# Kernel tuning notes

Hardware: AMD Instinct MI355X
Metric: run time of the kernel (lower is better)

The kernel has to match this reference:

```python
import jax, jax.numpy as jnp
import numpy as np

NUM_NODES = 50000
NUM_RELATIONS = 16
HIDDEN_DIM = 256
NUM_EDGES = 800000


def setup_inputs() -> dict:
    key = jax.random.key(0)
    k_x, k_ei, k_et, k_wr, k_ws, k_b = jax.random.split(key, 6)
    x = jax.random.normal(k_x, (NUM_NODES, HIDDEN_DIM), dtype=jnp.float32)
    edge_index = jax.random.randint(k_ei, (2, NUM_EDGES), 0, NUM_NODES, dtype=jnp.int64)
    edge_type = jax.random.randint(k_et, (NUM_EDGES,), 0, NUM_RELATIONS, dtype=jnp.int64)
    # Xavier-uniform-like scale for relation weights (fan_in=fan_out=d)
    lim = float(np.sqrt(6.0 / (HIDDEN_DIM + HIDDEN_DIM)))
    W_rel = jax.random.uniform(k_wr, (NUM_RELATIONS, HIDDEN_DIM, HIDDEN_DIM), minval=-lim, maxval=lim, dtype=jnp.float32)
    W_self = jax.random.uniform(k_ws, (HIDDEN_DIM, HIDDEN_DIM), minval=-lim, maxval=lim, dtype=jnp.float32)
    bias = jnp.zeros((HIDDEN_DIM,), dtype=jnp.float32)
    return {"x": x, "edge_index": edge_index, "edge_type": edge_type,
            "W_rel": W_rel, "W_self": W_self, "bias": bias}


def reference(x, edge_index, edge_type, W_rel, W_self, bias):
    # Transform every node under every relation: (N, R, d)
    xw = jnp.einsum('nd,rdh->nrh', x, W_rel)
    src = edge_index[0]
    dst = edge_index[1]
    # Per-edge messages: gather the (src, relation)-specific transform. (E, d)
    messages = xw[src, edge_type]
    # Scatter-add into destination nodes (sum over relations is implicit since
    # each edge carries exactly one relation and sums commute).
    agg = jax.ops.segment_sum(messages, dst, num_segments=NUM_NODES)
    out = agg + x @ W_self + bias
    return jax.nn.relu(out)
```

## Files before the change

kernel.cpp:

```cpp
#include <hip/hip_runtime.h>
#include <hip/hip_bf16.h>
#include <stdint.h>

#define D 256

typedef __attribute__((ext_vector_type(8))) short bf16x8;
typedef __attribute__((ext_vector_type(4))) float f32x4;
typedef __attribute__((ext_vector_type(4))) unsigned int u32x4;

#define GLOBAL_AS __attribute__((address_space(1)))
#define LDS_AS __attribute__((address_space(3)))

__device__ __forceinline__ unsigned short f2bf(float f) {
  union { float f; unsigned int u; } c; c.f = f;
  unsigned int r = (c.u + 0x7fffu + ((c.u >> 16) & 1u)) >> 16;
  return (unsigned short)r;
}
__device__ __forceinline__ float bf2f(unsigned short h) {
  union { unsigned int u; float f; } c; c.u = ((unsigned int)h) << 16;
  return c.f;
}

__global__ void convert_x_kernel(const float* __restrict__ x,
                                 unsigned short* __restrict__ xb, int n4) {
  int i = blockIdx.x * blockDim.x + threadIdx.x;
  if (i >= n4) return;
  float4 v = reinterpret_cast<const float4*>(x)[i];
  ushort4 o;
  o.x = f2bf(v.x); o.y = f2bf(v.y); o.z = f2bf(v.z); o.w = f2bf(v.w);
  reinterpret_cast<ushort4*>(xb)[i] = o;
}

__global__ void transpose_w_kernel(const float* __restrict__ Wrel,
                                   const float* __restrict__ Wself,
                                   unsigned short* __restrict__ Wt, int R) {
  __shared__ unsigned short tile[64][65];
  int r = blockIdx.z;
  const float* src = (r == R) ? Wself : (Wrel + (size_t)r * D * D);
  int d0 = blockIdx.x * 64, h0 = blockIdx.y * 64;
  for (int i = threadIdx.x; i < 64 * 64; i += blockDim.x) {
    int row = i >> 6, col = i & 63;
    tile[row][col] = f2bf(src[(size_t)(d0 + row) * D + h0 + col]);
  }
  __syncthreads();
  for (int i = threadIdx.x; i < 64 * 64; i += blockDim.x) {
    int row = i >> 6, col = i & 63;
    Wt[(size_t)r * D * D + (size_t)(h0 + row) * D + d0 + col] = tile[col][row];
  }
}

template <int MODE, int XB>
__global__ __launch_bounds__(256) void gemm_kernel(
    const unsigned short* __restrict__ Abf,
    const float* __restrict__ Af,
    const unsigned short* __restrict__ Bt,
    unsigned short* __restrict__ Cbf,
    float* __restrict__ Cf,
    const float* __restrict__ bias, int M, int ldc, int ntiles) {
  __shared__ unsigned short smem[128 * 128];
  unsigned short* As = smem;
  unsigned short* Bs = smem + 8192;

  const int tid = threadIdx.x;
  const int lane = tid & 63;
  const int wid = tid >> 6;
  const int wm = wid >> 1, wn = wid & 1;

  const int MBt = (M + 127) >> 7;
  const int PANEL = 8;
  const int per_panel = PANEL * ntiles;
  const int panel = blockIdx.x / per_panel;
  const int rem = blockIdx.x - panel * per_panel;
  const int pm0 = panel * PANEL;
  const int ph = min(PANEL, MBt - pm0);
  const int mi = pm0 + rem % ph;
  const int ni = rem / ph;
  const int m0 = mi * 128;
  const int n0 = ni * 128;

  f32x4 acc[4][4] = {};

  for (int k0 = 0; k0 < 256; k0 += 64) {
    __syncthreads();
    for (int i = 0; i < 4; ++i) {
      int chunk = i * 4 + wid;
      int row = chunk * 8 + (lane >> 3);
      int col = (lane & 7) * 8;
      const unsigned short* gb = Bt + (size_t)(n0 + row) * 256 + k0 + col;
      __builtin_amdgcn_global_load_lds((GLOBAL_AS void*)(void*)gb,
                                       (LDS_AS void*)(Bs + chunk * 512), 16, 0, 0);
    }
    if (XB) {
      for (int i = 0; i < 4; ++i) {
        int chunk = i * 4 + wid;
        int row = chunk * 8 + (lane >> 3);
        int col = (lane & 7) * 8;
        int ar = m0 + row; if (ar > M - 1) ar = M - 1;
        const unsigned short* ga = Abf + (size_t)ar * 256 + k0 + col;
        __builtin_amdgcn_global_load_lds((GLOBAL_AS void*)(void*)ga,
                                         (LDS_AS void*)(As + chunk * 512), 16, 0, 0);
      }
    } else {
      for (int i = 0; i < 8; ++i) {
        int idx = i * 256 + tid;
        int row = idx >> 4;
        int c4 = idx & 15;
        int ar = m0 + row; if (ar > M - 1) ar = M - 1;
        float4 v = *reinterpret_cast<const float4*>(Af + (size_t)ar * 256 + k0 + c4 * 4);
        ushort4 o;
        o.x = f2bf(v.x); o.y = f2bf(v.y); o.z = f2bf(v.z); o.w = f2bf(v.w);
        *reinterpret_cast<ushort4*>(&As[row * 64 + c4 * 4]) = o;
      }
    }
    __syncthreads();
    for (int kk = 0; kk < 2; ++kk) {
      bf16x8 af[4], bfr[4];
      int kof = kk * 32 + (lane >> 4) * 8;
      for (int mi2 = 0; mi2 < 4; ++mi2)
        af[mi2] = *(const bf16x8*)&As[(wm * 64 + mi2 * 16 + (lane & 15)) * 64 + kof];
      for (int ni2 = 0; ni2 < 4; ++ni2)
        bfr[ni2] = *(const bf16x8*)&Bs[(wn * 64 + ni2 * 16 + (lane & 15)) * 64 + kof];
      for (int mi2 = 0; mi2 < 4; ++mi2)
        for (int ni2 = 0; ni2 < 4; ++ni2)
          acc[mi2][ni2] = __builtin_amdgcn_mfma_f32_16x16x32_bf16(
              af[mi2], bfr[ni2], acc[mi2][ni2], 0, 0, 0);
    }
  }

  if (MODE == 1) {
    for (int mi2 = 0; mi2 < 4; ++mi2)
      for (int ni2 = 0; ni2 < 4; ++ni2) {
        int col = n0 + wn * 64 + ni2 * 16 + (lane & 15);
        int rbase = m0 + wm * 64 + mi2 * 16 + (lane >> 4) * 4;
        float b = bias[col];
        for (int j = 0; j < 4; ++j) {
          int row = rbase + j;
          if (row < M) Cf[(size_t)row * 256 + col] = acc[mi2][ni2][j] + b;
        }
      }
  } else {
    __syncthreads();
    for (int mi2 = 0; mi2 < 4; ++mi2)
      for (int ni2 = 0; ni2 < 4; ++ni2) {
        int colt = wn * 64 + ni2 * 16 + (lane & 15);
        int rbt = wm * 64 + mi2 * 16 + (lane >> 4) * 4;
        for (int j = 0; j < 4; ++j)
          smem[(rbt + j) * 128 + colt] = f2bf(acc[mi2][ni2][j]);
      }
    __syncthreads();
    for (int i = 0; i < 8; ++i) {
      int c = i * 256 + tid;
      int row = c >> 4;
      int cole = (c & 15) * 8;
      int grow = m0 + row;
      if (grow < M)
        *(u32x4*)&Cbf[(size_t)grow * ldc + n0 + cole] =
            *(const u32x4*)&smem[row * 128 + cole];
    }
  }
}

__global__ void hist_kernel(const int* __restrict__ ei, const int* __restrict__ et,
                            int* __restrict__ counts, int E, int M, int R, int RB) {
  for (int i = blockIdx.x * blockDim.x + threadIdx.x; i < E;
       i += gridDim.x * blockDim.x) {
    int dst = min(max(ei[E + i], 0), M - 1);
    int rel = min(max(et[i], 0), R - 1);
    int b = rel / RB;
    atomicAdd(&counts[b * M + dst], 1);
  }
}

__global__ void scan1_kernel(const int* __restrict__ counts, int* __restrict__ bsum,
                             int NBINS) {
  __shared__ int red[256];
  int i = blockIdx.x * 256 + threadIdx.x;
  red[threadIdx.x] = (i < NBINS) ? counts[i] : 0;
  __syncthreads();
  for (int s = 128; s > 0; s >>= 1) {
    if (threadIdx.x < s) red[threadIdx.x] += red[threadIdx.x + s];
    __syncthreads();
  }
  if (threadIdx.x == 0) bsum[blockIdx.x] = red[0];
}

__global__ void scan2_kernel(int* __restrict__ bsum, int NB) {
  __shared__ int sh[1024];
  int t = threadIdx.x;
  int v = (t < NB) ? bsum[t] : 0;
  sh[t] = v;
  __syncthreads();
  for (int off = 1; off < 1024; off <<= 1) {
    int u = (t >= off) ? sh[t - off] : 0;
    __syncthreads();
    sh[t] += u;
    __syncthreads();
  }
  if (t < NB) bsum[t] = sh[t] - v;
}

__global__ void scan3_kernel(const int* __restrict__ counts, const int* __restrict__ bsum,
                             int* __restrict__ offs, int NBINS) {
  __shared__ int sh[256];
  int b = blockIdx.x, t = threadIdx.x;
  int i = b * 256 + t;
  int v = (i < NBINS) ? counts[i] : 0;
  sh[t] = v;
  __syncthreads();
  for (int off = 1; off < 256; off <<= 1) {
    int u = (t >= off) ? sh[t - off] : 0;
    __syncthreads();
    sh[t] += u;
    __syncthreads();
  }
  int excl = sh[t] - v + bsum[b];
  if (i < NBINS) offs[i] = excl;
  if (i == NBINS - 1) offs[NBINS] = excl + v;
}

__global__ void fill_kernel(const int* __restrict__ ei, const int* __restrict__ et,
                            const int* __restrict__ offs, int* __restrict__ cursor,
                            int* __restrict__ ev, int E, int M, int R, int RB) {
  for (int i = blockIdx.x * blockDim.x + threadIdx.x; i < E;
       i += gridDim.x * blockDim.x) {
    int dst = min(max(ei[E + i], 0), M - 1);
    int src = min(max(ei[i], 0), M - 1);
    int rel = min(max(et[i], 0), R - 1);
    int b = rel / RB;
    int bin = b * M + dst;
    int p = atomicAdd(&cursor[bin], 1);
    ev[offs[bin] + p] = src * RB + (rel - b * RB);
  }
}

template <int RELU>
__global__ void gather_kernel(const int* __restrict__ offs, const int* __restrict__ ev,
                              const unsigned short* __restrict__ xw,
                              float* __restrict__ out, int M, int base) {
  int w = blockIdx.x * (blockDim.x >> 6) + (threadIdx.x >> 6);
  int lane = threadIdx.x & 63;
  if (w >= M) return;
  int beg = offs[base + w], end = offs[base + w + 1];
  float a0 = 0, a1 = 0, a2 = 0, a3 = 0;
  int s = beg;
  for (; s + 3 < end; s += 4) {
    int v0 = ev[s], v1 = ev[s + 1], v2 = ev[s + 2], v3 = ev[s + 3];
    ushort4 t0 = *((const ushort4*)(xw + ((size_t)v0 << 8)) + lane);
    ushort4 t1 = *((const ushort4*)(xw + ((size_t)v1 << 8)) + lane);
    ushort4 t2 = *((const ushort4*)(xw + ((size_t)v2 << 8)) + lane);
    ushort4 t3 = *((const ushort4*)(xw + ((size_t)v3 << 8)) + lane);
    a0 += bf2f(t0.x) + bf2f(t1.x) + bf2f(t2.x) + bf2f(t3.x);
    a1 += bf2f(t0.y) + bf2f(t1.y) + bf2f(t2.y) + bf2f(t3.y);
    a2 += bf2f(t0.z) + bf2f(t1.z) + bf2f(t2.z) + bf2f(t3.z);
    a3 += bf2f(t0.w) + bf2f(t1.w) + bf2f(t2.w) + bf2f(t3.w);
  }
  for (; s < end; ++s) {
    int v = ev[s];
    ushort4 t = *((const ushort4*)(xw + ((size_t)v << 8)) + lane);
    a0 += bf2f(t.x); a1 += bf2f(t.y); a2 += bf2f(t.z); a3 += bf2f(t.w);
  }
  if (RELU || end > beg) {
    float4* o = (float4*)(out + (size_t)w * 256) + lane;
    float4 cur = *o;
    cur.x += a0; cur.y += a1; cur.z += a2; cur.w += a3;
    if (RELU) {
      cur.x = fmaxf(cur.x, 0.f); cur.y = fmaxf(cur.y, 0.f);
      cur.z = fmaxf(cur.z, 0.f); cur.w = fmaxf(cur.w, 0.f);
    }
    *o = cur;
  }
}

__global__ void relu_kernel(float* __restrict__ out, int n4) {
  int i = blockIdx.x * blockDim.x + threadIdx.x;
  if (i >= n4) return;
  float4 v = reinterpret_cast<float4*>(out)[i];
  v.x = fmaxf(v.x, 0.f); v.y = fmaxf(v.y, 0.f);
  v.z = fmaxf(v.z, 0.f); v.w = fmaxf(v.w, 0.f);
  reinterpret_cast<float4*>(out)[i] = v;
}

__global__ void fb_self_kernel(const float* __restrict__ x,
                               const float* __restrict__ Wself,
                               const float* __restrict__ bias,
                               float* __restrict__ out, int M) {
  int w = blockIdx.x * (blockDim.x >> 6) + (threadIdx.x >> 6);
  int lane = threadIdx.x & 63;
  int nw = gridDim.x * (blockDim.x >> 6);
  for (int n = w; n < M; n += nw) {
    float a0 = 0, a1 = 0, a2 = 0, a3 = 0;
    const float* xr = x + (size_t)n * 256;
    for (int d = 0; d < 256; ++d) {
      float xv = xr[d];
      float4 wv = *reinterpret_cast<const float4*>(Wself + (size_t)d * 256 + lane * 4);
      a0 = fmaf(xv, wv.x, a0); a1 = fmaf(xv, wv.y, a1);
      a2 = fmaf(xv, wv.z, a2); a3 = fmaf(xv, wv.w, a3);
    }
    float4 b = *reinterpret_cast<const float4*>(bias + lane * 4);
    float4 o = {a0 + b.x, a1 + b.y, a2 + b.z, a3 + b.w};
    *reinterpret_cast<float4*>(out + (size_t)n * 256 + lane * 4) = o;
  }
}

__global__ void fb_edge_kernel(const int* __restrict__ ei, const int* __restrict__ et,
                               const float* __restrict__ x,
                               const float* __restrict__ Wrel,
                               float* __restrict__ out, int E, int M, int R) {
  int w = blockIdx.x * (blockDim.x >> 6) + (threadIdx.x >> 6);
  int lane = threadIdx.x & 63;
  int nw = gridDim.x * (blockDim.x >> 6);
  for (int e = w; e < E; e += nw) {
    int src = min(max(ei[e], 0), M - 1);
    int dst = min(max(ei[E + e], 0), M - 1);
    int rel = min(max(et[e], 0), R - 1);
    const float* xr = x + (size_t)src * 256;
    const float* W = Wrel + (size_t)rel * 256 * 256;
    float a0 = 0, a1 = 0, a2 = 0, a3 = 0;
    for (int d = 0; d < 256; ++d) {
      float xv = xr[d];
      float4 wv = *reinterpret_cast<const float4*>(W + (size_t)d * 256 + lane * 4);
      a0 = fmaf(xv, wv.x, a0); a1 = fmaf(xv, wv.y, a1);
      a2 = fmaf(xv, wv.z, a2); a3 = fmaf(xv, wv.w, a3);
    }
    float* o = out + (size_t)dst * 256 + lane * 4;
    atomicAdd(o + 0, a0);
    atomicAdd(o + 1, a1);
    atomicAdd(o + 2, a2);
    atomicAdd(o + 3, a3);
  }
}

extern "C" void kernel_launch(void* const* d_in, const int* in_sizes, int n_in,
                              void* d_out, int out_size, void* d_ws, size_t ws_size,
                              hipStream_t stream) {
  const float* x = (const float*)d_in[0];
  const int* ei = (const int*)d_in[1];
  const int* et = (const int*)d_in[2];
  const float* Wrel = (const float*)d_in[3];
  const float* Wself = (const float*)d_in[4];
  const float* bias = (const float*)d_in[5];
  float* out = (float*)d_out;

  const int M = in_sizes[0] / D;
  const int E = in_sizes[1] / 2;
  const int R = in_sizes[3] / (D * D);

  const int MB = (M + 127) / 128;
  const int n4 = M * D / 4;

  const size_t wtElems = (size_t)(R + 1) * D * D;
  const size_t xbElems = (size_t)M * D;
  const size_t yElems = (size_t)M * D;

  int use_xb = 0, RB = 0, nb = 0;
  size_t nbM = 0, NB2 = 0;
  for (int pass = 0; pass < 2 && RB == 0; ++pass) {
    for (int rb = R; rb >= 1; rb >>= 1) {
      int nbc = (R + rb - 1) / rb;
      size_t nbm = (size_t)nbc * M;
      size_t nb2 = (nbm + 255) / 256;
      if (nb2 > 1024) continue;
      size_t ib = (3 * nbm + 1 + nb2 + (size_t)E) * 4;
      if (ws_size < ib + 512) continue;
      size_t bfA = (ws_size - ib - 512) / 2;
      size_t need = wtElems + (pass == 0 ? xbElems : 0) + 512 + yElems * (size_t)rb;
      if (need <= bfA) {
        use_xb = (pass == 0); RB = rb; nb = nbc; nbM = nbm; NB2 = nb2;
        break;
      }
    }
  }

  if (RB == 0) {
    fb_self_kernel<<<2048, 256, 0, stream>>>(x, Wself, bias, out, M);
    fb_edge_kernel<<<2048, 256, 0, stream>>>(ei, et, x, Wrel, out, E, M, R);
    relu_kernel<<<(n4 + 255) / 256, 256, 0, stream>>>(out, n4);
    return;
  }

  int* counts = (int*)d_ws;
  int* cursor = counts + nbM;
  int* offs = cursor + nbM;
  int* bsum = offs + nbM + 1;
  int* ev = bsum + NB2;
  uintptr_t bfp = (uintptr_t)(ev + E);
  bfp = (bfp + 255) & ~(uintptr_t)255;
  unsigned short* Wt = (unsigned short*)bfp;
  unsigned short* xb = Wt + wtElems;
  size_t off = wtElems + (use_xb ? xbElems : 0);
  off = (off + 255) & ~(size_t)255;
  unsigned short* xw = Wt + off;

  hipMemsetAsync(counts, 0, 2 * nbM * 4, stream);
  hist_kernel<<<1024, 256, 0, stream>>>(ei, et, counts, E, M, R, RB);
  scan1_kernel<<<(int)NB2, 256, 0, stream>>>(counts, bsum, (int)nbM);
  scan2_kernel<<<1, 1024, 0, stream>>>(bsum, (int)NB2);
  scan3_kernel<<<(int)NB2, 256, 0, stream>>>(counts, bsum, offs, (int)nbM);
  fill_kernel<<<1024, 256, 0, stream>>>(ei, et, offs, cursor, ev, E, M, R, RB);

  transpose_w_kernel<<<dim3(4, 4, R + 1), 256, 0, stream>>>(Wrel, Wself, Wt, R);
  if (use_xb)
    convert_x_kernel<<<(n4 + 255) / 256, 256, 0, stream>>>(x, xb, n4);

  if (use_xb)
    gemm_kernel<1, 1><<<MB * 2, 256, 0, stream>>>(
        xb, nullptr, Wt + (size_t)R * D * D, nullptr, out, bias, M, 256, 2);
  else
    gemm_kernel<1, 0><<<MB * 2, 256, 0, stream>>>(
        nullptr, x, Wt + (size_t)R * D * D, nullptr, out, bias, M, 256, 2);

  for (int b = 0; b < nb; ++b) {
    int rlo = b * RB;
    int rbw = min(RB, R - rlo);
    const unsigned short* BtB = Wt + (size_t)rlo * D * D;
    if (use_xb)
      gemm_kernel<0, 1><<<MB * rbw * 2, 256, 0, stream>>>(
          xb, nullptr, BtB, xw, nullptr, nullptr, M, rbw * 256, rbw * 2);
    else
      gemm_kernel<0, 0><<<MB * rbw * 2, 256, 0, stream>>>(
          nullptr, x, BtB, xw, nullptr, nullptr, M, rbw * 256, rbw * 2);
    if (b == nb - 1)
      gather_kernel<1><<<(M + 3) / 4, 256, 0, stream>>>(offs, ev, xw, out, M, b * M);
    else
      gather_kernel<0><<<(M + 3) / 4, 256, 0, stream>>>(offs, ev, xw, out, M, b * M);
  }
}
```

Before: 517.6 us.

## Fuse self-loop GEMM into relation GEMM with 256-row tiles and 512 threads

Merges the separate W_self GEMM launch into the first relation-block GEMM by giving extra column tiles the self weights and the bias epilogue. It also enlarges the M tile from 128 to 256 rows, using 8 waves per block, so each B tile loaded into shared memory is reused across twice as many rows. The bf16 output epilogue is staged in two halves to fit the LDS buffer. In exchange, the LDS footprint is larger and each block holds more waves, which can reduce occupancy.

```diff
diff --git a/kernel.cpp b/kernel.cpp
--- a/kernel.cpp
+++ b/kernel.cpp
@@ -49,24 +49,27 @@
   }
 }
 
-template <int MODE, int XB>
-__global__ __launch_bounds__(256) void gemm_kernel(
+template <int XB>
+__global__ __launch_bounds__(512) void gemm_kernel(
     const unsigned short* __restrict__ Abf,
     const float* __restrict__ Af,
     const unsigned short* __restrict__ Bt,
+    const unsigned short* __restrict__ Bself,
     unsigned short* __restrict__ Cbf,
     float* __restrict__ Cf,
-    const float* __restrict__ bias, int M, int ldc, int ntiles) {
-  __shared__ unsigned short smem[128 * 128];
+    const float* __restrict__ bias,
+    int M, int ldc, int ntiles, int nxw) {
+  __shared__ unsigned short smem[256 * 64 + 128 * 64];
   unsigned short* As = smem;
-  unsigned short* Bs = smem + 8192;
+  unsigned short* Bs = smem + 256 * 64;
 
   const int tid = threadIdx.x;
   const int lane = tid & 63;
   const int wid = tid >> 6;
-  const int wm = wid >> 1, wn = wid & 1;
-
-  const int MBt = (M + 127) >> 7;
+  const int wm = wid >> 1;
+  const int wn = wid & 1;
+
+  const int MBt = (M + 255) >> 8;
   const int PANEL = 8;
   const int per_panel = PANEL * ntiles;
   const int panel = blockIdx.x / per_panel;
@@ -75,24 +78,29 @@
   const int ph = min(PANEL, MBt - pm0);
   const int mi = pm0 + rem % ph;
   const int ni = rem / ph;
-  const int m0 = mi * 128;
-  const int n0 = ni * 128;
+  const int m0 = mi * 256;
+
+  const bool self = (ni >= nxw);
+  const int n0 = self ? 0 : ni * 128;
+  const int scol0 = self ? (ni - nxw) * 128 : 0;
+  const unsigned short* Bsrc = self ? (Bself + (size_t)scol0 * 256)
+                                    : (Bt + (size_t)n0 * 256);
 
   f32x4 acc[4][4] = {};
 
   for (int k0 = 0; k0 < 256; k0 += 64) {
     __syncthreads();
-    for (int i = 0; i < 4; ++i) {
-      int chunk = i * 4 + wid;
+    for (int i = 0; i < 2; ++i) {
+      int chunk = i * 8 + wid;
       int row = chunk * 8 + (lane >> 3);
       int col = (lane & 7) * 8;
-      const unsigned short* gb = Bt + (size_t)(n0 + row) * 256 + k0 + col;
+      const unsigned short* gb = Bsrc + (size_t)row * 256 + k0 + col;
       __builtin_amdgcn_global_load_lds((GLOBAL_AS void*)(void*)gb,
                                        (LDS_AS void*)(Bs + chunk * 512), 16, 0, 0);
     }
     if (XB) {
       for (int i = 0; i < 4; ++i) {
-        int chunk = i * 4 + wid;
+        int chunk = i * 8 + wid;
         int row = chunk * 8 + (lane >> 3);
         int col = (lane & 7) * 8;
         int ar = m0 + row; if (ar > M - 1) ar = M - 1;
@@ -101,15 +109,19 @@
                                          (LDS_AS void*)(As + chunk * 512), 16, 0, 0);
       }
     } else {
-      for (int i = 0; i < 8; ++i) {
-        int idx = i * 256 + tid;
-        int row = idx >> 4;
-        int c4 = idx & 15;
+      for (int i = 0; i < 4; ++i) {
+        int idx = i * 512 + tid;
+        int row = idx >> 3;
+        int c8 = idx & 7;
         int ar = m0 + row; if (ar > M - 1) ar = M - 1;
-        float4 v = *reinterpret_cast<const float4*>(Af + (size_t)ar * 256 + k0 + c4 * 4);
-        ushort4 o;
-        o.x = f2bf(v.x); o.y = f2bf(v.y); o.z = f2bf(v.z); o.w = f2bf(v.w);
-        *reinterpret_cast<ushort4*>(&As[row * 64 + c4 * 4]) = o;
+        const float* src = Af + (size_t)ar * 256 + k0 + c8 * 8;
+        float4 v0 = *reinterpret_cast<const float4*>(src);
+        float4 v1 = *reinterpret_cast<const float4*>(src + 4);
+        ushort4 o0, o1;
+        o0.x = f2bf(v0.x); o0.y = f2bf(v0.y); o0.z = f2bf(v0.z); o0.w = f2bf(v0.w);
+        o1.x = f2bf(v1.x); o1.y = f2bf(v1.y); o1.z = f2bf(v1.z); o1.w = f2bf(v1.w);
+        *reinterpret_cast<ushort4*>(&As[row * 64 + c8 * 8]) = o0;
+        *reinterpret_cast<ushort4*>(&As[row * 64 + c8 * 8 + 4]) = o1;
       }
     }
     __syncthreads();
@@ -127,10 +139,10 @@
     }
   }
 
-  if (MODE == 1) {
+  if (self) {
     for (int mi2 = 0; mi2 < 4; ++mi2)
       for (int ni2 = 0; ni2 < 4; ++ni2) {
-        int col = n0 + wn * 64 + ni2 * 16 + (lane & 15);
+        int col = scol0 + wn * 64 + ni2 * 16 + (lane & 15);
         int rbase = m0 + wm * 64 + mi2 * 16 + (lane >> 4) * 4;
         float b = bias[col];
         for (int j = 0; j < 4; ++j) {
@@ -139,23 +151,27 @@
         }
       }
   } else {
-    __syncthreads();
-    for (int mi2 = 0; mi2 < 4; ++mi2)
-      for (int ni2 = 0; ni2 < 4; ++ni2) {
-        int colt = wn * 64 + ni2 * 16 + (lane & 15);
-        int rbt = wm * 64 + mi2 * 16 + (lane >> 4) * 4;
-        for (int j = 0; j < 4; ++j)
-          smem[(rbt + j) * 128 + colt] = f2bf(acc[mi2][ni2][j]);
-      }
-    __syncthreads();
-    for (int i = 0; i < 8; ++i) {
-      int c = i * 256 + tid;
-      int row = c >> 4;
-      int cole = (c & 15) * 8;
-      int grow = m0 + row;
-      if (grow < M)
-        *(u32x4*)&Cbf[(size_t)grow * ldc + n0 + cole] =
-            *(const u32x4*)&smem[row * 128 + cole];
+    for (int h = 0; h < 2; ++h) {
+      __syncthreads();
+      for (int u = 0; u < 2; ++u) {
+        int mi2 = h * 2 + u;
+        for (int ni2 = 0; ni2 < 4; ++ni2) {
+          int col = wn * 64 + ni2 * 16 + (lane & 15);
+          int lr0 = wm * 32 + u * 16 + (lane >> 4) * 4;
+          for (int j = 0; j < 4; ++j)
+            smem[(lr0 + j) * 128 + col] = f2bf(acc[mi2][ni2][j]);
+        }
+      }
+      __syncthreads();
+      for (int i = 0; i < 4; ++i) {
+        int c = i * 512 + tid;
+        int row = c >> 4;
+        int cole = (c & 15) * 8;
+        int grow = m0 + (row >> 5) * 64 + h * 32 + (row & 31);
+        if (grow < M)
+          *(u32x4*)&Cbf[(size_t)grow * ldc + n0 + cole] =
+              *(const u32x4*)&smem[row * 128 + cole];
+      }
     }
   }
 }
@@ -345,7 +361,6 @@
   const int E = in_sizes[1] / 2;
   const int R = in_sizes[3] / (D * D);
 
-  const int MB = (M + 127) / 128;
   const int n4 = M * D / 4;
 
   const size_t wtElems = (size_t)(R + 1) * D * D;
@@ -390,6 +405,7 @@
   size_t off = wtElems + (use_xb ? xbElems : 0);
   off = (off + 255) & ~(size_t)255;
   unsigned short* xw = Wt + off;
+  unsigned short* WtSelf = Wt + (size_t)R * D * D;
 
   hipMemsetAsync(counts, 0, 2 * nbM * 4, stream);
   hist_kernel<<<1024, 256, 0, stream>>>(ei, et, counts, E, M, R, RB);
@@ -402,23 +418,20 @@
   if (use_xb)
     convert_x_kernel<<<(n4 + 255) / 256, 256, 0, stream>>>(x, xb, n4);
 
-  if (use_xb)
-    gemm_kernel<1, 1><<<MB * 2, 256, 0, stream>>>(
-        xb, nullptr, Wt + (size_t)R * D * D, nullptr, out, bias, M, 256, 2);
-  else
-    gemm_kernel<1, 0><<<MB * 2, 256, 0, stream>>>(
-        nullptr, x, Wt + (size_t)R * D * D, nullptr, out, bias, M, 256, 2);
-
+  const int MBt = (M + 255) / 256;
   for (int b = 0; b < nb; ++b) {
     int rlo = b * RB;
     int rbw = min(RB, R - rlo);
+    int nxw = rbw * 2;
+    int nself = (b == 0) ? 2 : 0;
+    int ntiles = nxw + nself;
     const unsigned short* BtB = Wt + (size_t)rlo * D * D;
     if (use_xb)
-      gemm_kernel<0, 1><<<MB * rbw * 2, 256, 0, stream>>>(
-          xb, nullptr, BtB, xw, nullptr, nullptr, M, rbw * 256, rbw * 2);
+      gemm_kernel<1><<<MBt * ntiles, 512, 0, stream>>>(
+          xb, nullptr, BtB, WtSelf, xw, out, bias, M, rbw * 256, ntiles, nxw);
     else
-      gemm_kernel<0, 0><<<MB * rbw * 2, 256, 0, stream>>>(
-          nullptr, x, BtB, xw, nullptr, nullptr, M, rbw * 256, rbw * 2);
+      gemm_kernel<0><<<MBt * ntiles, 512, 0, stream>>>(
+          nullptr, x, BtB, WtSelf, xw, out, bias, M, rbw * 256, ntiles, nxw);
     if (b == nb - 1)
       gather_kernel<1><<<(M + 3) / 4, 256, 0, stream>>>(offs, ev, xw, out, M, b * M);
     else
```

Result: slower. 598.3 us (+15.6%).

## Aggregate neighbor features per relation before transforming with one fused-K GEMM

Applied to the files above, without the earlier changes.

The order of work is swapped. Before, every node was transformed under every relation, all those results were stored, and edge messages were gathered from them. Now bf16 source features are summed per (destination, relation) bin into a wide Z matrix with the node's own features appended. One GEMM then runs with K concatenated across relations plus the self weight, adding bias and applying ReLU in its epilogue. This removes the large per-relation xw intermediate and the random gathers from it, in exchange for a finer (dst, rel) CSR sort and a large Z buffer that is written and then re-read.

```diff
diff --git a/kernel.cpp b/kernel.cpp
--- a/kernel.cpp
+++ b/kernel.cpp
@@ -6,7 +6,6 @@
 
 typedef __attribute__((ext_vector_type(8))) short bf16x8;
 typedef __attribute__((ext_vector_type(4))) float f32x4;
-typedef __attribute__((ext_vector_type(4))) unsigned int u32x4;
 
 #define GLOBAL_AS __attribute__((address_space(1)))
 #define LDS_AS __attribute__((address_space(3)))
@@ -31,12 +30,16 @@
   reinterpret_cast<ushort4*>(xb)[i] = o;
 }
 
-__global__ void transpose_w_kernel(const float* __restrict__ Wrel,
-                                   const float* __restrict__ Wself,
-                                   unsigned short* __restrict__ Wt, int R) {
+__global__ void transpose_w2_kernel(const float* __restrict__ Wrel,
+                                    const float* __restrict__ Wself,
+                                    unsigned short* __restrict__ Wt2,
+                                    int R, int RBZ, int KB) {
   __shared__ unsigned short tile[64][65];
   int r = blockIdx.z;
   const float* src = (r == R) ? Wself : (Wrel + (size_t)r * D * D);
+  int b, kbase;
+  if (r == R) { b = 0; kbase = min(RBZ, R) * 256; }
+  else { b = r / RBZ; kbase = (r - b * RBZ) * 256; }
   int d0 = blockIdx.x * 64, h0 = blockIdx.y * 64;
   for (int i = threadIdx.x; i < 64 * 64; i += blockDim.x) {
     int row = i >> 6, col = i & 63;
@@ -45,19 +48,142 @@
   __syncthreads();
   for (int i = threadIdx.x; i < 64 * 64; i += blockDim.x) {
     int row = i >> 6, col = i & 63;
-    Wt[(size_t)r * D * D + (size_t)(h0 + row) * D + d0 + col] = tile[col][row];
-  }
-}
-
-template <int MODE, int XB>
-__global__ __launch_bounds__(256) void gemm_kernel(
-    const unsigned short* __restrict__ Abf,
-    const float* __restrict__ Af,
+    Wt2[((size_t)b * 256 + h0 + row) * KB + kbase + d0 + col] = tile[col][row];
+  }
+}
+
+__global__ void hist_kernel(const int* __restrict__ ei, const int* __restrict__ et,
+                            int* __restrict__ counts, int E, int M, int R) {
+  for (int i = blockIdx.x * blockDim.x + threadIdx.x; i < E;
+       i += gridDim.x * blockDim.x) {
+    int dst = min(max(ei[E + i], 0), M - 1);
+    int rel = min(max(et[i], 0), R - 1);
+    atomicAdd(&counts[dst * R + rel], 1);
+  }
+}
+
+__global__ void scan1_kernel(const int* __restrict__ counts, int* __restrict__ bsum,
+                             int NBINS) {
+  __shared__ int red[256];
+  int t = threadIdx.x;
+  int base = blockIdx.x * 1024 + t * 4;
+  int s = 0;
+  if (base < NBINS) {
+    int4 c = *reinterpret_cast<const int4*>(&counts[base]);
+    s = c.x + c.y + c.z + c.w;
+  }
+  red[t] = s;
+  __syncthreads();
+  for (int st = 128; st > 0; st >>= 1) {
+    if (t < st) red[t] += red[t + st];
+    __syncthreads();
+  }
+  if (t == 0) bsum[blockIdx.x] = red[0];
+}
+
+__global__ void scan2_kernel(int* __restrict__ bsum, int NB) {
+  __shared__ int sh[1024];
+  int t = threadIdx.x;
+  int v = (t < NB) ? bsum[t] : 0;
+  sh[t] = v;
+  __syncthreads();
+  for (int off = 1; off < 1024; off <<= 1) {
+    int u = (t >= off) ? sh[t - off] : 0;
+    __syncthreads();
+    sh[t] += u;
+    __syncthreads();
+  }
+  if (t < NB) bsum[t] = sh[t] - v;
+}
+
+__global__ void scan3_kernel(const int* __restrict__ counts, const int* __restrict__ bsum,
+                             int* __restrict__ offs, int NBINS) {
+  __shared__ int sh[256];
+  int t = threadIdx.x;
+  int base = blockIdx.x * 1024 + t * 4;
+  int c0 = 0, c1 = 0, c2 = 0, c3 = 0;
+  if (base < NBINS) {
+    int4 c = *reinterpret_cast<const int4*>(&counts[base]);
+    c0 = c.x; c1 = c.y; c2 = c.z; c3 = c.w;
+  }
+  int s = c0 + c1 + c2 + c3;
+  sh[t] = s;
+  __syncthreads();
+  for (int off = 1; off < 256; off <<= 1) {
+    int u = (t >= off) ? sh[t - off] : 0;
+    __syncthreads();
+    sh[t] += u;
+    __syncthreads();
+  }
+  int excl = sh[t] - s + bsum[blockIdx.x];
+  if (base < NBINS) {
+    offs[base] = excl;
+    offs[base + 1] = excl + c0;
+    offs[base + 2] = excl + c0 + c1;
+    offs[base + 3] = excl + c0 + c1 + c2;
+    if (base + 4 == NBINS) offs[NBINS] = excl + s;
+  }
+}
+
+__global__ void fill_kernel(const int* __restrict__ ei, const int* __restrict__ et,
+                            const int* __restrict__ offs, int* __restrict__ cursor,
+                            int* __restrict__ ev, int E, int M, int R) {
+  for (int i = blockIdx.x * blockDim.x + threadIdx.x; i < E;
+       i += gridDim.x * blockDim.x) {
+    int dst = min(max(ei[E + i], 0), M - 1);
+    int src = min(max(ei[i], 0), M - 1);
+    int rel = min(max(et[i], 0), R - 1);
+    int bin = dst * R + rel;
+    int p = atomicAdd(&cursor[bin], 1);
+    ev[offs[bin] + p] = src;
+  }
+}
+
+template <int FIRST>
+__global__ void agg_kernel(const int* __restrict__ offs, const int* __restrict__ ev,
+                           const unsigned short* __restrict__ xb,
+                           unsigned short* __restrict__ z,
+                           int M, int R, int rlo, int rbw, int ZLD) {
+  int w = blockIdx.x * (blockDim.x >> 6) + (threadIdx.x >> 6);
+  int lane = threadIdx.x & 63;
+  if (w >= M) return;
+  const int binBase = w * R + rlo;
+  unsigned short* zr = z + (size_t)w * ZLD;
+  for (int rl = 0; rl < rbw; ++rl) {
+    int beg = offs[binBase + rl], end = offs[binBase + rl + 1];
+    float a0 = 0, a1 = 0, a2 = 0, a3 = 0;
+    int s = beg;
+    for (; s + 1 < end; s += 2) {
+      int v0 = ev[s], v1 = ev[s + 1];
+      ushort4 t0 = *((const ushort4*)(xb + ((size_t)v0 << 8)) + lane);
+      ushort4 t1 = *((const ushort4*)(xb + ((size_t)v1 << 8)) + lane);
+      a0 += bf2f(t0.x) + bf2f(t1.x);
+      a1 += bf2f(t0.y) + bf2f(t1.y);
+      a2 += bf2f(t0.z) + bf2f(t1.z);
+      a3 += bf2f(t0.w) + bf2f(t1.w);
+    }
+    if (s < end) {
+      ushort4 t = *((const ushort4*)(xb + ((size_t)ev[s] << 8)) + lane);
+      a0 += bf2f(t.x); a1 += bf2f(t.y); a2 += bf2f(t.z); a3 += bf2f(t.w);
+    }
+    ushort4 o;
+    o.x = f2bf(a0); o.y = f2bf(a1); o.z = f2bf(a2); o.w = f2bf(a3);
+    *((ushort4*)(zr + rl * 256) + lane) = o;
+  }
+  if (FIRST) {
+    ushort4 t = *((const ushort4*)(xb + ((size_t)w << 8)) + lane);
+    *((ushort4*)(zr + rbw * 256) + lane) = t;
+  }
+}
+
+template <int FIRST, int LAST>
+__global__ __launch_bounds__(256) void gemm_z_kernel(
+    const unsigned short* __restrict__ A,
     const unsigned short* __restrict__ Bt,
-    unsigned short* __restrict__ Cbf,
-    float* __restrict__ Cf,
-    const float* __restrict__ bias, int M, int ldc, int ntiles) {
-  __shared__ unsigned short smem[128 * 128];
+    float* __restrict__ out,
+    const float* __restrict__ bias,
+    int M, int ZLD, int KB, int kTotal) {
+  __shared__ unsigned short smem[128 * 64 * 2];
   unsigned short* As = smem;
   unsigned short* Bs = smem + 8192;
 
@@ -67,12 +193,11 @@
   const int wm = wid >> 1, wn = wid & 1;
 
   const int MBt = (M + 127) >> 7;
-  const int PANEL = 8;
-  const int per_panel = PANEL * ntiles;
+  const int per_panel = 16;
   const int panel = blockIdx.x / per_panel;
   const int rem = blockIdx.x - panel * per_panel;
-  const int pm0 = panel * PANEL;
-  const int ph = min(PANEL, MBt - pm0);
+  const int pm0 = panel * 8;
+  const int ph = min(8, MBt - pm0);
   const int mi = pm0 + rem % ph;
   const int ni = rem / ph;
   const int m0 = mi * 128;
@@ -80,37 +205,24 @@
 
   f32x4 acc[4][4] = {};
 
-  for (int k0 = 0; k0 < 256; k0 += 64) {
+  for (int k0 = 0; k0 < kTotal; k0 += 64) {
     __syncthreads();
     for (int i = 0; i < 4; ++i) {
       int chunk = i * 4 + wid;
       int row = chunk * 8 + (lane >> 3);
       int col = (lane & 7) * 8;
-      const unsigned short* gb = Bt + (size_t)(n0 + row) * 256 + k0 + col;
+      const unsigned short* gb = Bt + (size_t)(n0 + row) * KB + k0 + col;
       __builtin_amdgcn_global_load_lds((GLOBAL_AS void*)(void*)gb,
                                        (LDS_AS void*)(Bs + chunk * 512), 16, 0, 0);
     }
-    if (XB) {
-      for (int i = 0; i < 4; ++i) {
-        int chunk = i * 4 + wid;
-        int row = chunk * 8 + (lane >> 3);
-        int col = (lane & 7) * 8;
-        int ar = m0 + row; if (ar > M - 1) ar = M - 1;
-        const unsigned short* ga = Abf + (size_t)ar * 256 + k0 + col;
-        __builtin_amdgcn_global_load_lds((GLOBAL_AS void*)(void*)ga,
-                                         (LDS_AS void*)(As + chunk * 512), 16, 0, 0);
-      }
-    } else {
-      for (int i = 0; i < 8; ++i) {
-        int idx = i * 256 + tid;
-        int row = idx >> 4;
-        int c4 = idx & 15;
-        int ar = m0 + row; if (ar > M - 1) ar = M - 1;
-        float4 v = *reinterpret_cast<const float4*>(Af + (size_t)ar * 256 + k0 + c4 * 4);
-        ushort4 o;
-        o.x = f2bf(v.x); o.y = f2bf(v.y); o.z = f2bf(v.z); o.w = f2bf(v.w);
-        *reinterpret_cast<ushort4*>(&As[row * 64 + c4 * 4]) = o;
-      }
+    for (int i = 0; i < 4; ++i) {
+      int chunk = i * 4 + wid;
+      int row = chunk * 8 + (lane >> 3);
+      int col = (lane & 7) * 8;
+      int ar = m0 + row; if (ar > M - 1) ar = M - 1;
+      const unsigned short* ga = A + (size_t)ar * ZLD + k0 + col;
+      __builtin_amdgcn_global_load_lds((GLOBAL_AS void*)(void*)ga,
+                                       (LDS_AS void*)(As + chunk * 512), 16, 0, 0);
     }
     __syncthreads();
     for (int kk = 0; kk < 2; ++kk) {
@@ -127,148 +239,21 @@
     }
   }
 
-  if (MODE == 1) {
-    for (int mi2 = 0; mi2 < 4; ++mi2)
-      for (int ni2 = 0; ni2 < 4; ++ni2) {
-        int col = n0 + wn * 64 + ni2 * 16 + (lane & 15);
-        int rbase = m0 + wm * 64 + mi2 * 16 + (lane >> 4) * 4;
-        float b = bias[col];
-        for (int j = 0; j < 4; ++j) {
-          int row = rbase + j;
-          if (row < M) Cf[(size_t)row * 256 + col] = acc[mi2][ni2][j] + b;
+  for (int mi2 = 0; mi2 < 4; ++mi2)
+    for (int ni2 = 0; ni2 < 4; ++ni2) {
+      int col = n0 + wn * 64 + ni2 * 16 + (lane & 15);
+      int rbase = m0 + wm * 64 + mi2 * 16 + (lane >> 4) * 4;
+      float b = FIRST ? bias[col] : 0.f;
+      for (int j = 0; j < 4; ++j) {
+        int row = rbase + j;
+        if (row < M) {
+          float v = acc[mi2][ni2][j] + b;
+          if (!FIRST) v += out[(size_t)row * 256 + col];
+          if (LAST) v = fmaxf(v, 0.f);
+          out[(size_t)row * 256 + col] = v;
         }
       }
-  } else {
-    __syncthreads();
-    for (int mi2 = 0; mi2 < 4; ++mi2)
-      for (int ni2 = 0; ni2 < 4; ++ni2) {
-        int colt = wn * 64 + ni2 * 16 + (lane & 15);
-        int rbt = wm * 64 + mi2 * 16 + (lane >> 4) * 4;
-        for (int j = 0; j < 4; ++j)
-          smem[(rbt + j) * 128 + colt] = f2bf(acc[mi2][ni2][j]);
-      }
-    __syncthreads();
-    for (int i = 0; i < 8; ++i) {
-      int c = i * 256 + tid;
-      int row = c >> 4;
-      int cole = (c & 15) * 8;
-      int grow = m0 + row;
-      if (grow < M)
-        *(u32x4*)&Cbf[(size_t)grow * ldc + n0 + cole] =
-            *(const u32x4*)&smem[row * 128 + cole];
-    }
-  }
-}
-
-__global__ void hist_kernel(const int* __restrict__ ei, const int* __restrict__ et,
-                            int* __restrict__ counts, int E, int M, int R, int RB) {
-  for (int i = blockIdx.x * blockDim.x + threadIdx.x; i < E;
-       i += gridDim.x * blockDim.x) {
-    int dst = min(max(ei[E + i], 0), M - 1);
-    int rel = min(max(et[i], 0), R - 1);
-    int b = rel / RB;
-    atomicAdd(&counts[b * M + dst], 1);
-  }
-}
-
-__global__ void scan1_kernel(const int* __restrict__ counts, int* __restrict__ bsum,
-                             int NBINS) {
-  __shared__ int red[256];
-  int i = blockIdx.x * 256 + threadIdx.x;
-  red[threadIdx.x] = (i < NBINS) ? counts[i] : 0;
-  __syncthreads();
-  for (int s = 128; s > 0; s >>= 1) {
-    if (threadIdx.x < s) red[threadIdx.x] += red[threadIdx.x + s];
-    __syncthreads();
-  }
-  if (threadIdx.x == 0) bsum[blockIdx.x] = red[0];
-}
-
-__global__ void scan2_kernel(int* __restrict__ bsum, int NB) {
-  __shared__ int sh[1024];
-  int t = threadIdx.x;
-  int v = (t < NB) ? bsum[t] : 0;
-  sh[t] = v;
-  __syncthreads();
-  for (int off = 1; off < 1024; off <<= 1) {
-    int u = (t >= off) ? sh[t - off] : 0;
-    __syncthreads();
-    sh[t] += u;
-    __syncthreads();
-  }
-  if (t < NB) bsum[t] = sh[t] - v;
-}
-
-__global__ void scan3_kernel(const int* __restrict__ counts, const int* __restrict__ bsum,
-                             int* __restrict__ offs, int NBINS) {
-  __shared__ int sh[256];
-  int b = blockIdx.x, t = threadIdx.x;
-  int i = b * 256 + t;
-  int v = (i < NBINS) ? counts[i] : 0;
-  sh[t] = v;
-  __syncthreads();
-  for (int off = 1; off < 256; off <<= 1) {
-    int u = (t >= off) ? sh[t - off] : 0;
-    __syncthreads();
-    sh[t] += u;
-    __syncthreads();
-  }
-  int excl = sh[t] - v + bsum[b];
-  if (i < NBINS) offs[i] = excl;
-  if (i == NBINS - 1) offs[NBINS] = excl + v;
-}
-
-__global__ void fill_kernel(const int* __restrict__ ei, const int* __restrict__ et,
-                            const int* __restrict__ offs, int* __restrict__ cursor,
-                            int* __restrict__ ev, int E, int M, int R, int RB) {
-  for (int i = blockIdx.x * blockDim.x + threadIdx.x; i < E;
-       i += gridDim.x * blockDim.x) {
-    int dst = min(max(ei[E + i], 0), M - 1);
-    int src = min(max(ei[i], 0), M - 1);
-    int rel = min(max(et[i], 0), R - 1);
-    int b = rel / RB;
-    int bin = b * M + dst;
-    int p = atomicAdd(&cursor[bin], 1);
-    ev[offs[bin] + p] = src * RB + (rel - b * RB);
-  }
-}
-
-template <int RELU>
-__global__ void gather_kernel(const int* __restrict__ offs, const int* __restrict__ ev,
-                              const unsigned short* __restrict__ xw,
-                              float* __restrict__ out, int M, int base) {
-  int w = blockIdx.x * (blockDim.x >> 6) + (threadIdx.x >> 6);
-  int lane = threadIdx.x & 63;
-  if (w >= M) return;
-  int beg = offs[base + w], end = offs[base + w + 1];
-  float a0 = 0, a1 = 0, a2 = 0, a3 = 0;
-  int s = beg;
-  for (; s + 3 < end; s += 4) {
-    int v0 = ev[s], v1 = ev[s + 1], v2 = ev[s + 2], v3 = ev[s + 3];
-    ushort4 t0 = *((const ushort4*)(xw + ((size_t)v0 << 8)) + lane);
-    ushort4 t1 = *((const ushort4*)(xw + ((size_t)v1 << 8)) + lane);
-    ushort4 t2 = *((const ushort4*)(xw + ((size_t)v2 << 8)) + lane);
-    ushort4 t3 = *((const ushort4*)(xw + ((size_t)v3 << 8)) + lane);
-    a0 += bf2f(t0.x) + bf2f(t1.x) + bf2f(t2.x) + bf2f(t3.x);
-    a1 += bf2f(t0.y) + bf2f(t1.y) + bf2f(t2.y) + bf2f(t3.y);
-    a2 += bf2f(t0.z) + bf2f(t1.z) + bf2f(t2.z) + bf2f(t3.z);
-    a3 += bf2f(t0.w) + bf2f(t1.w) + bf2f(t2.w) + bf2f(t3.w);
-  }
-  for (; s < end; ++s) {
-    int v = ev[s];
-    ushort4 t = *((const ushort4*)(xw + ((size_t)v << 8)) + lane);
-    a0 += bf2f(t.x); a1 += bf2f(t.y); a2 += bf2f(t.z); a3 += bf2f(t.w);
-  }
-  if (RELU || end > beg) {
-    float4* o = (float4*)(out + (size_t)w * 256) + lane;
-    float4 cur = *o;
-    cur.x += a0; cur.y += a1; cur.z += a2; cur.w += a3;
-    if (RELU) {
-      cur.x = fmaxf(cur.x, 0.f); cur.y = fmaxf(cur.y, 0.f);
-      cur.z = fmaxf(cur.z, 0.f); cur.w = fmaxf(cur.w, 0.f);
-    }
-    *o = cur;
-  }
+    }
 }
 
 __global__ void relu_kernel(float* __restrict__ out, int n4) {
@@ -345,83 +330,72 @@
   const int E = in_sizes[1] / 2;
   const int R = in_sizes[3] / (D * D);
 
-  const int MB = (M + 127) / 128;
   const int n4 = M * D / 4;
-
-  const size_t wtElems = (size_t)(R + 1) * D * D;
-  const size_t xbElems = (size_t)M * D;
-  const size_t yElems = (size_t)M * D;
-
-  int use_xb = 0, RB = 0, nb = 0;
-  size_t nbM = 0, NB2 = 0;
-  for (int pass = 0; pass < 2 && RB == 0; ++pass) {
-    for (int rb = R; rb >= 1; rb >>= 1) {
-      int nbc = (R + rb - 1) / rb;
-      size_t nbm = (size_t)nbc * M;
-      size_t nb2 = (nbm + 255) / 256;
-      if (nb2 > 1024) continue;
-      size_t ib = (3 * nbm + 1 + nb2 + (size_t)E) * 4;
-      if (ws_size < ib + 512) continue;
-      size_t bfA = (ws_size - ib - 512) / 2;
-      size_t need = wtElems + (pass == 0 ? xbElems : 0) + 512 + yElems * (size_t)rb;
-      if (need <= bfA) {
-        use_xb = (pass == 0); RB = rb; nb = nbc; nbM = nbm; NB2 = nb2;
-        break;
-      }
-    }
-  }
-
-  if (RB == 0) {
+  const size_t NBINS = (size_t)M * R;
+  const size_t NB2 = (NBINS + 1023) / 1024;
+  const size_t intBytes = (4 * NBINS + 1 + NB2 + (size_t)E) * 4;
+
+  int RBZ = 0, nb = 0;
+  if (NB2 <= 1024) {
+    for (int rbz = R; rbz >= 1; --rbz) {
+      int nbc = (R + rbz - 1) / rbz;
+      size_t KB = (size_t)(rbz + 1) * 256;
+      size_t elems = (size_t)nbc * 256 * KB
+                   + (size_t)M * 256
+                   + (size_t)M * KB;
+      if (intBytes + 512 + 2 * elems <= ws_size) { RBZ = rbz; nb = nbc; break; }
+    }
+  }
+
+  if (RBZ == 0) {
     fb_self_kernel<<<2048, 256, 0, stream>>>(x, Wself, bias, out, M);
     fb_edge_kernel<<<2048, 256, 0, stream>>>(ei, et, x, Wrel, out, E, M, R);
     relu_kernel<<<(n4 + 255) / 256, 256, 0, stream>>>(out, n4);
     return;
   }
 
+  const int KB = (RBZ + 1) * 256;
+
   int* counts = (int*)d_ws;
-  int* cursor = counts + nbM;
-  int* offs = cursor + nbM;
-  int* bsum = offs + nbM + 1;
+  int* cursor = counts + NBINS;
+  int* offs = cursor + NBINS;
+  int* bsum = offs + NBINS + 1;
   int* ev = bsum + NB2;
   uintptr_t bfp = (uintptr_t)(ev + E);
   bfp = (bfp + 255) & ~(uintptr_t)255;
-  unsigned short* Wt = (unsigned short*)bfp;
-  unsigned short* xb = Wt + wtElems;
-  size_t off = wtElems + (use_xb ? xbElems : 0);
-  off = (off + 255) & ~(size_t)255;
-  unsigned short* xw = Wt + off;
-
-  hipMemsetAsync(counts, 0, 2 * nbM * 4, stream);
-  hist_kernel<<<1024, 256, 0, stream>>>(ei, et, counts, E, M, R, RB);
-  scan1_kernel<<<(int)NB2, 256, 0, stream>>>(counts, bsum, (int)nbM);
+  unsigned short* Wt2 = (unsigned short*)bfp;
+  unsigned short* xb = Wt2 + (size_t)nb * 256 * KB;
+  unsigned short* z = xb + (size_t)M * 256;
+
+  hipMemsetAsync(counts, 0, 2 * NBINS * 4, stream);
+  hist_kernel<<<1024, 256, 0, stream>>>(ei, et, counts, E, M, R);
+  scan1_kernel<<<(int)NB2, 256, 0, stream>>>(counts, bsum, (int)NBINS);
   scan2_kernel<<<1, 1024, 0, stream>>>(bsum, (int)NB2);
-  scan3_kernel<<<(int)NB2, 256, 0, stream>>>(counts, bsum, offs, (int)nbM);
-  fill_kernel<<<1024, 256, 0, stream>>>(ei, et, offs, cursor, ev, E, M, R, RB);
-
-  transpose_w_kernel<<<dim3(4, 4, R + 1), 256, 0, stream>>>(Wrel, Wself, Wt, R);
-  if (use_xb)
-    convert_x_kernel<<<(n4 + 255) / 256, 256, 0, stream>>>(x, xb, n4);
-
-  if (use_xb)
-    gemm_kernel<1, 1><<<MB * 2, 256, 0, stream>>>(
-        xb, nullptr, Wt + (size_t)R * D * D, nullptr, out, bias, M, 256, 2);
-  else
-    gemm_kernel<1, 0><<<MB * 2, 256, 0, stream>>>(
-        nullptr, x, Wt + (size_t)R * D * D, nullptr, out, bias, M, 256, 2);
-
+  scan3_kernel<<<(int)NB2, 256, 0, stream>>>(counts, bsum, offs, (int)NBINS);
+  fill_kernel<<<1024, 256, 0, stream>>>(ei, et, offs, cursor, ev, E, M, R);
+
+  transpose_w2_kernel<<<dim3(4, 4, R + 1), 256, 0, stream>>>(Wrel, Wself, Wt2, R, RBZ, KB);
+  convert_x_kernel<<<(n4 + 255) / 256, 256, 0, stream>>>(x, xb, n4);
+
+  const int MBt = (M + 127) / 128;
+  const int aggGrid = (M + 3) / 4;
   for (int b = 0; b < nb; ++b) {
-    int rlo = b * RB;
-    int rbw = min(RB, R - rlo);
-    const unsigned short* BtB = Wt + (size_t)rlo * D * D;
-    if (use_xb)
-      gemm_kernel<0, 1><<<MB * rbw * 2, 256, 0, stream>>>(
-          xb, nullptr, BtB, xw, nullptr, nullptr, M, rbw * 256, rbw * 2);
+    int rlo = b * RBZ;
+    int rbw = min(RBZ, R - rlo);
+    bool first = (b == 0), last = (b == nb - 1);
+    if (first)
+      agg_kernel<1><<<aggGrid, 256, 0, stream>>>(offs, ev, xb, z, M, R, rlo, rbw, KB);
     else
-      gemm_kernel<0, 0><<<MB * rbw * 2, 256, 0, stream>>>(
-          nullptr, x, BtB, xw, nullptr, nullptr, M, rbw * 256, rbw * 2);
-    if (b == nb - 1)
-      gather_kernel<1><<<(M + 3) / 4, 256, 0, stream>>>(offs, ev, xw, out, M, b * M);
+      agg_kernel<0><<<aggGrid, 256, 0, stream>>>(offs, ev, xb, z, M, R, rlo, rbw, KB);
+    int kTot = rbw * 256 + (first ? 256 : 0);
+    const unsigned short* Bt = Wt2 + (size_t)b * 256 * KB;
+    if (first && last)
+      gemm_z_kernel<1, 1><<<MBt * 2, 256, 0, stream>>>(z, Bt, out, bias, M, KB, KB, kTot);
+    else if (first)
+      gemm_z_kernel<1, 0><<<MBt * 2, 256, 0, stream>>>(z, Bt, out, bias, M, KB, KB, kTot);
+    else if (last)
+      gemm_z_kernel<0, 1><<<MBt * 2, 256, 0, stream>>>(z, Bt, out, bias, M, KB, KB, kTot);
     else
-      gather_kernel<0><<<(M + 3) / 4, 256, 0, stream>>>(offs, ev, xw, out, M, b * M);
-  }
-}
+      gemm_z_kernel<0, 0><<<MBt * 2, 256, 0, stream>>>(z, Bt, out, bias, M, KB, KB, kTot);
+  }
+}
```

Measured after the change: 711.7 us. +37.5%, slower.
